# Kernel optimization log

Measured on AMD Instinct MI355X. Metric: run time of the kernel, lower is better.

Reference implementation:

```python
import jax, jax.numpy as jnp
import numpy as np

N_NODES = 100000


def gcn_conv(h, src, dst, n_nodes):
    """One GCNConv propagation with self-loops and symmetric normalization.
    h: [N, D] already linearly transformed node features.
    src, dst: [E2] int32/int64 edge endpoints (self-loops already appended).
    """
    deg = jnp.zeros((n_nodes,), h.dtype).at[dst].add(jnp.ones_like(dst, dtype=h.dtype))
    dinv = jnp.where(deg > 0, jax.lax.rsqrt(deg), 0.0)  # deg^{-1/2}, 0 for isolated
    norm = dinv[src] * dinv[dst]                         # [E2]
    msgs = norm[:, None] * h[src]                        # gather + scale
    return jnp.zeros((n_nodes, h.shape[1]), h.dtype).at[dst].add(msgs)


def setup_inputs() -> dict:
    key = jax.random.key(0)
    k1, k2, k3, k4 = jax.random.split(key, 4)
    F_IN, HID, N_CLS, N_EDGES = 512, 16, 64, 3200000
    x = jax.random.normal(k1, (N_NODES, F_IN), dtype=jnp.float32)
    edge_index = jax.random.randint(k2, (2, N_EDGES), 0, N_NODES, dtype=jnp.int64)
    W1 = jax.random.normal(k3, (F_IN, HID), dtype=jnp.float32) * (1.0 / np.sqrt(F_IN))
    b1 = jnp.zeros((HID,), jnp.float32)
    W2 = jax.random.normal(k4, (HID, N_CLS), dtype=jnp.float32) * (1.0 / np.sqrt(HID))
    b2 = jnp.zeros((N_CLS,), jnp.float32)
    return {"x": x, "edge_index": edge_index, "W1": W1, "b1": b1, "W2": W2, "b2": b2}


def reference(x, edge_index, W1, b1, W2, b2):
    n = x.shape[0]
    loops = jnp.arange(n, dtype=edge_index.dtype)
    src = jnp.concatenate([edge_index[0], loops])
    dst = jnp.concatenate([edge_index[1], loops])
    # layer 1: transform -> propagate -> bias -> relu (dropout is identity in eval)
    h = gcn_conv(x @ W1, src, dst, n) + b1
    h = jax.nn.relu(h)
    # layer 2
    out = gcn_conv(h @ W2, src, dst, n) + b2
    return out
```

## Files before the change

kernel.cpp:

```cpp
#include <hip/hip_runtime.h>

typedef unsigned short u16;
typedef unsigned int u32;

#define FIN 512
#define HID 16
#define NCLS 64

#define NBSH 7
#define BUCK (1 << NBSH)
#define SENTS ((1u << 25) - 1u)

typedef __bf16 bf16x8 __attribute__((ext_vector_type(8)));
typedef float f32x4 __attribute__((ext_vector_type(4)));

__device__ __forceinline__ float bf2f_raw(u16 u) {
    u32 x = ((u32)u) << 16;
    float f; __builtin_memcpy(&f, &x, 4); return f;
}
__device__ __forceinline__ float ldf(const void* p, long long i, int f32) {
    return f32 ? ((const float*)p)[i] : bf2f_raw(((const u16*)p)[i]);
}
__device__ __forceinline__ u16 f2bf_rne(float v) {
    u32 bits; __builtin_memcpy(&bits, &v, 4);
    u32 lsb = (bits >> 16) & 1;
    bits += 0x7FFFu + lsb;
    return (u16)(bits >> 16);
}

__global__ void k_probe(const void* x, const void* w1, const int* eidx, int E,
                        int* flags) {
    __shared__ int nz_x, nz_w, weird_x, weird_w, odd_nz;
    if (threadIdx.x == 0) { nz_x = 0; nz_w = 0; weird_x = 0; weird_w = 0; odd_nz = 0; }
    __syncthreads();
    const u16* xu = (const u16*)x;
    const u16* wu = (const u16*)w1;
    for (int i = threadIdx.x; i < 8192; i += 256) {
        u16 u = xu[i];
        if (u) atomicOr(&nz_x, 1);
        int e = (u >> 7) & 0xff;
        if ((e == 0 && (u & 0x7f)) || e >= 0xC0) atomicAdd(&weird_x, 1);
        u16 w = wu[i];
        if (w) atomicOr(&nz_w, 1);
        int ew = (w >> 7) & 0xff;
        if ((ew == 0 && (w & 0x7f)) || ew >= 0xC0) atomicAdd(&weird_w, 1);
    }
    int lim = (2 * E < 4096) ? 2 * E : 4096;
    for (int i = 1 + 2 * (int)threadIdx.x; i < lim; i += 512) {
        if (eidx[i] != 0) atomicOr(&odd_nz, 1);
    }
    __syncthreads();
    if (threadIdx.x == 0) {
        flags[0] = (odd_nz == 0) ? 1 : 0;
        flags[1] = (weird_x > 64) ? 1 : 0;
        flags[2] = (weird_w > 64) ? 1 : 0;
        flags[3] = (nz_x == 0) ? 1 : 0;
        flags[4] = (nz_w == 0) ? 1 : 0;
    }
}

__device__ __forceinline__ int ld_src(const int* eidx, int E, int e, int f64) {
    return f64 ? eidx[2LL * e] : eidx[e];
}
__device__ __forceinline__ int ld_dst(const int* eidx, int E, int e, int f64) {
    return f64 ? eidx[2LL * E + 2LL * e] : eidx[(long long)E + e];
}

__global__ void k_binA(const int* eidx, const int* flags, int* bcnt8,
                       int E, int n, int nbuck, int nblocks) {
    extern __shared__ int lcnt[];
    int tid = threadIdx.x;
    for (int i = tid; i < nbuck; i += 256) lcnt[i] = 0;
    __syncthreads();
    int f64 = flags[0];
    long long stride = (long long)nblocks * 256;
    for (long long e = (long long)blockIdx.x * 256 + tid; e < E; e += stride) {
        int d = ld_dst(eidx, E, (int)e, f64);
        if ((unsigned)d < (unsigned)n) atomicAdd(&lcnt[d >> NBSH], 1);
    }
    __syncthreads();
    int sub = blockIdx.x & 7;
    for (int i = tid; i < nbuck; i += 256) {
        int v = lcnt[i];
        if (v) atomicAdd(&bcnt8[i * 8 + sub], v);
    }
}

__global__ void k_scanb(const int* bcnt8, int* boff, int* cursor8, int NSUB) {
    __shared__ int part[1024];
    int t = threadIdx.x;
    int K = (NSUB + 1023) >> 10;
    long long base = (long long)t * K;
    int local = 0;
    for (int j = 0; j < K; j++) {
        long long idx = base + j;
        if (idx < NSUB) local += bcnt8[idx];
    }
    part[t] = local;
    __syncthreads();
    for (int s = 1; s < 1024; s <<= 1) {
        int u = (t >= s) ? part[t - s] : 0;
        __syncthreads();
        part[t] += u;
        __syncthreads();
    }
    int acc = part[t] - local;
    for (int j = 0; j < K; j++) {
        long long idx = base + j;
        if (idx < NSUB) {
            int v = bcnt8[idx];
            boff[idx] = acc;
            cursor8[idx] = acc;
            acc += v;
        }
    }
    if (t == 1023) boff[NSUB] = part[1023];
}

__global__ void k_binB(const int* eidx, const int* flags, int* cursor8,
                       u32* pairs, int E, int n, int nblocks) {
    int f64 = flags[0];
    int sub = blockIdx.x & 7;
    long long stride = (long long)nblocks * 256;
    for (long long e = (long long)blockIdx.x * 256 + threadIdx.x; e < E; e += stride) {
        int d = ld_dst(eidx, E, (int)e, f64);
        if ((unsigned)d >= (unsigned)n) continue;
        int s = ld_src(eidx, E, (int)e, f64);
        u32 su = ((unsigned)s < (unsigned)n) ? (u32)s : SENTS;
        int slot = atomicAdd(&cursor8[(d >> NBSH) * 8 + sub], 1);
        pairs[slot] = ((u32)(d & (BUCK - 1)) << 25) | su;
    }
}

__global__ void __launch_bounds__(256)
k_csrb(const u32* pairs, const int* boff, float* dinv, int* row_start,
       int* csr, int n, int nbuck) {
    __shared__ int cnt[BUCK];
    __shared__ int ex[BUCK];
    __shared__ int cur[BUCK];
    int b = blockIdx.x, tid = threadIdx.x;
    for (int i = tid; i < BUCK; i += 256) cnt[i] = 0;
    __syncthreads();
    int beg = boff[b * 8], end = boff[b * 8 + 8];
    for (int i = beg + tid; i < end; i += 256) atomicAdd(&cnt[pairs[i] >> 25], 1);
    __syncthreads();
    if (tid < BUCK) ex[tid] = cnt[tid];
    __syncthreads();
    for (int s = 1; s < BUCK; s <<= 1) {
        int u = (tid >= s && tid < BUCK) ? ex[tid - s] : 0;
        __syncthreads();
        if (tid < BUCK) ex[tid] += u;
        __syncthreads();
    }
    int base = b << NBSH;
    if (tid < BUCK) {
        int e0 = ex[tid] - cnt[tid];
        cur[tid] = e0;
        int node = base + tid;
        if (node < n) {
            row_start[node] = beg + e0;
            dinv[node] = rsqrtf((float)cnt[tid] + 1.0f);
        }
    }
    if (b == nbuck - 1 && tid == 0) row_start[n] = boff[nbuck * 8];
    __syncthreads();
    for (int i = beg + tid; i < end; i += 256) {
        u32 pr = pairs[i];
        int dl = pr >> 25;
        u32 s = pr & SENTS;
        int slot = atomicAdd(&cur[dl], 1);
        csr[beg + slot] = (s < (unsigned)n) ? (int)s : -1;
    }
}

__global__ void __launch_bounds__(256)
k_gemm1(const void* x, const void* w1, const int* flags, const float* dinv,
        float* h0s, int n) {
    __shared__ __attribute__((aligned(16))) u16 w1t[16 * 512];
    int tid = threadIdx.x;
    int fx = flags[1], fw = flags[2];
    for (int i = tid; i < 8192; i += 256) {
        int k = i >> 4, f = i & 15;
        float v = ldf(w1, (long long)k * HID + f, fw);
        int idx = ((f << 9) + k) ^ ((f & 7) << 3);
        w1t[idx] = f2bf_rne(v);
    }
    __syncthreads();

    int wave = tid >> 6;
    int lane = tid & 63;
    int base = blockIdx.x * 64 + wave * 16;
    if (base >= n) return;
    int rowA = base + (lane & 15);
    if (rowA >= n) rowA = n - 1;
    int g = lane >> 4;
    int nn = lane & 15;
    f32x4 acc = {0.0f, 0.0f, 0.0f, 0.0f};

    if (!fx) {
        const u16* xp = (const u16*)x + (long long)rowA * FIN + g * 8;
        #pragma unroll
        for (int kb = 0; kb < FIN; kb += 32) {
            bf16x8 a = *(const bf16x8*)(xp + kb);
            int bidx = ((nn << 9) + kb + g * 8) ^ ((nn & 7) << 3);
            bf16x8 b = *(const bf16x8*)(w1t + bidx);
            acc = __builtin_amdgcn_mfma_f32_16x16x32_bf16(a, b, acc, 0, 0, 0);
        }
    } else {
        const float* xp = (const float*)x + (long long)rowA * FIN + g * 8;
        #pragma unroll 4
        for (int kb = 0; kb < FIN; kb += 32) {
            float vf[8];
            *(float4*)(vf) = *(const float4*)(xp + kb);
            *(float4*)(vf + 4) = *(const float4*)(xp + kb + 4);
            bf16x8 a;
            #pragma unroll
            for (int j = 0; j < 8; j++) ((u16*)&a)[j] = f2bf_rne(vf[j]);
            int bidx = ((nn << 9) + kb + g * 8) ^ ((nn & 7) << 3);
            bf16x8 b = *(const bf16x8*)(w1t + bidx);
            acc = __builtin_amdgcn_mfma_f32_16x16x32_bf16(a, b, acc, 0, 0, 0);
        }
    }
    #pragma unroll
    for (int r = 0; r < 4; r++) {
        int node = base + g * 4 + r;
        if (node < n) h0s[node * HID + nn] = acc[r] * dinv[node];
    }
}

template <int RELU>
__global__ void k_gather(const int* row_start, const int* csr, const float* dinv,
                         const float* h_in, const void* b, const int* flags,
                         float* h_out, int n) {
    int t = blockIdx.x * 256 + threadIdx.x;
    if (t >= n * 4) return;
    int d = t >> 2;
    int g = t & 3;
    int beg = row_start[d], end = row_start[d + 1];
    const float4* hv = (const float4*)h_in;
    float4 acc = hv[d * 4 + g];
    #pragma unroll 4
    for (int i = beg; i < end; i++) {
        int s = csr[i];
        if (s >= 0) {
            float4 v = hv[s * 4 + g];
            acc.x += v.x; acc.y += v.y; acc.z += v.z; acc.w += v.w;
        }
    }
    float di = dinv[d];
    float4 o;
    if (RELU) {
        int fw = flags[2];
        o.x = di * fmaxf(di * acc.x + ldf(b, g * 4 + 0, fw), 0.0f);
        o.y = di * fmaxf(di * acc.y + ldf(b, g * 4 + 1, fw), 0.0f);
        o.z = di * fmaxf(di * acc.z + ldf(b, g * 4 + 2, fw), 0.0f);
        o.w = di * fmaxf(di * acc.w + ldf(b, g * 4 + 3, fw), 0.0f);
    } else {
        o.x = di * acc.x; o.y = di * acc.y; o.z = di * acc.z; o.w = di * acc.w;
    }
    ((float4*)h_out)[t] = o;
}

__global__ void k_check(const int* eidx, const float* h0s, const float* g,
                        int* flags, int E, int n) {
    __shared__ int h0nz, gnz, dstz;
    if (threadIdx.x == 0) { h0nz = 0; gnz = 0; dstz = 0; }
    __syncthreads();
    for (int i = threadIdx.x; i < 4096; i += 256) {
        if (h0s[i] != 0.0f) atomicOr(&h0nz, 1);
        if (g[i] != 0.0f) atomicOr(&gnz, 1);
    }
    int f64 = flags[0];
    for (int e = threadIdx.x; e < 2048; e += 256) {
        if (ld_dst(eidx, E, e, f64) == 0) atomicAdd(&dstz, 1);
    }
    __syncthreads();
    if (threadIdx.x == 0) {
        int b0 = flags[3];
        int b1 = flags[4];
        int b2 = (dstz > 102);
        int b3 = (h0nz == 0);
        int b4 = (gnz == 0);
        int b5 = flags[1];
        int b6 = flags[2];
        int b7 = flags[0];
        flags[9] = b0 | (b1 << 1) | (b2 << 2) | (b3 << 3) | (b4 << 4) |
                   (b5 << 5) | (b6 << 6) | (b7 << 7);
        flags[8] = (b0 | b1 | b2 | b3 | b4) ? 1 : 0;
    }
}

__global__ void SimplifiedGCN_5574867550498_kernel(
        const float* g, const void* w2, const void* b2, const int* flags,
        float* out, int n) {
    int t = blockIdx.x * 256 + threadIdx.x;
    if (t >= n * NCLS) return;
    int node = t >> 6;
    int c = t & 63;
    int fw = flags[2];
    float acc = ldf(b2, c, fw);
    for (int k = 0; k < HID; k++) {
        acc += g[node * HID + k] * ldf(w2, (long long)k * NCLS + c, fw);
    }
    if (t == 0 && flags[8]) acc = 4096.0f + 2.0f * (float)flags[9];
    out[t] = acc;
}

extern "C" void kernel_launch(void* const* d_in, const int* in_sizes, int n_in,
                              void* d_out, int out_size, void* d_ws, size_t ws_size,
                              hipStream_t stream) {
    const void* x = d_in[0];
    const int* eidx = (const int*)d_in[1];
    const void* w1 = d_in[2];
    const void* b1 = d_in[3];
    const void* w2 = d_in[4];
    const void* b2 = d_in[5];
    float* out = (float*)d_out;

    int n = in_sizes[0] / FIN;
    int E = in_sizes[1] / 2;
    int total_out = n * NCLS;
    int nb_out = (total_out + 255) / 256;
    size_t out_bytes = (size_t)total_out * 4;

    hipMemsetAsync(d_out, 0x42, out_bytes, stream);

    if (n <= 0 || E <= 0 || n_in < 6) {
        hipMemsetAsync(d_out, 0x4E, out_bytes, stream);
        return;
    }
    if (n >= (1 << 25)) {
        hipMemsetAsync(d_out, 0x4B, out_bytes, stream);
        return;
    }

    int nbuck = (n + BUCK - 1) >> NBSH;
    int NSUB = nbuck * 8;

    size_t A = 255;
    size_t o_flags = 0;
    size_t o_dinv  = 256;
    size_t o_h0s   = o_dinv + (((size_t)n * 4 + A) & ~A);
    size_t o_h2ps  = o_h0s  + (((size_t)n * HID * 4 + A) & ~A);
    size_t o_g     = o_h2ps + (((size_t)n * HID * 4 + A) & ~A);
    size_t o_bcnt  = o_g    + (((size_t)n * HID * 4 + A) & ~A);
    size_t o_boff  = o_bcnt + (((size_t)NSUB * 4 + A) & ~A);
    size_t o_cur   = o_boff + (((size_t)(NSUB + 1) * 4 + A) & ~A);
    size_t o_rs    = o_cur  + (((size_t)NSUB * 4 + A) & ~A);
    size_t o_pairs = o_rs   + (((size_t)(n + 1) * 4 + A) & ~A);
    size_t o_csr   = o_pairs + (((size_t)E * 4 + A) & ~A);
    size_t need    = o_csr  + (((size_t)E * 4 + A) & ~A);

    if (ws_size < need) {
        hipMemsetAsync(d_out, 0x4A, out_bytes, stream);
        return;
    }

    char* p = (char*)d_ws;
    int* flags     = (int*)(p + o_flags);
    float* dinv    = (float*)(p + o_dinv);
    float* h0s     = (float*)(p + o_h0s);
    float* h2ps    = (float*)(p + o_h2ps);
    float* g       = (float*)(p + o_g);
    int* bcnt8     = (int*)(p + o_bcnt);
    int* boff      = (int*)(p + o_boff);
    int* cursor8   = (int*)(p + o_cur);
    int* row_start = (int*)(p + o_rs);
    u32* pairs     = (u32*)(p + o_pairs);
    int* csr       = (int*)(p + o_csr);

    int nb_g1 = (n + 63) / 64;
    int nb_h4 = (n * 4 + 255) / 256;
    int nbA = 512, nbB = 1024;

    k_probe<<<1, 256, 0, stream>>>(x, w1, eidx, E, flags);
    hipMemsetAsync(bcnt8, 0, (size_t)NSUB * 4, stream);
    k_binA<<<nbA, 256, (size_t)nbuck * 4, stream>>>(eidx, flags, bcnt8, E, n,
                                                    nbuck, nbA);
    k_scanb<<<1, 1024, 0, stream>>>(bcnt8, boff, cursor8, NSUB);
    k_binB<<<nbB, 256, 0, stream>>>(eidx, flags, cursor8, pairs, E, n, nbB);
    k_csrb<<<nbuck, 256, 0, stream>>>(pairs, boff, dinv, row_start, csr, n, nbuck);
    k_gemm1<<<nb_g1, 256, 0, stream>>>(x, w1, flags, dinv, h0s, n);
    k_gather<1><<<nb_h4, 256, 0, stream>>>(row_start, csr, dinv, h0s, b1, flags,
                                           h2ps, n);
    k_gather<0><<<nb_h4, 256, 0, stream>>>(row_start, csr, dinv, h2ps, b1, flags,
                                           g, n);
    k_check<<<1, 256, 0, stream>>>(eidx, h0s, g, flags, E, n);
    SimplifiedGCN_5574867550498_kernel<<<nb_out, 256, 0, stream>>>(
        g, w2, b2, flags, out, n);
}
```

Before: 712.7 us.

## Replace global atomic bucket cursors with per-block LDS cursors and larger buckets

Edge binning now gives each block a contiguous edge range and a per-(bucket, block) count matrix, so the scan produces exact per-block offsets. Scatter then uses LDS atomics instead of contended global atomics. Buckets grow from 128 to 1024 nodes, so the CSR build runs fewer, larger blocks of 1024 threads, and the pair packing shifts to 22 source bits. The cost is a larger count matrix (about 50k entries) for the single-block scan to process, plus a lower limit on node count.

New measurement: 669.8 us. 1.06x faster.

```diff
diff --git a/kernel.cpp b/kernel.cpp
--- a/kernel.cpp
+++ b/kernel.cpp
@@ -7,9 +7,10 @@
 #define HID 16
 #define NCLS 64
 
-#define NBSH 7
+#define NBSH 10
 #define BUCK (1 << NBSH)
-#define SENTS ((1u << 25) - 1u)
+#define NBLK 512
+#define SENTS ((1u << 22) - 1u)
 
 typedef __bf16 bf16x8 __attribute__((ext_vector_type(8)));
 typedef float f32x4 __attribute__((ext_vector_type(4)));
@@ -65,28 +66,31 @@
 __device__ __forceinline__ int ld_dst(const int* eidx, int E, int e, int f64) {
     return f64 ? eidx[2LL * E + 2LL * e] : eidx[(long long)E + e];
 }
-
-__global__ void k_binA(const int* eidx, const int* flags, int* bcnt8,
-                       int E, int n, int nbuck, int nblocks) {
+__device__ __forceinline__ void blk_range(int E, int bid, int* e0, int* e1) {
+    *e0 = (int)((long long)E * bid / NBLK);
+    *e1 = (int)((long long)E * (bid + 1) / NBLK);
+}
+
+__global__ void __launch_bounds__(512)
+k_binA(const int* eidx, const int* flags, int* bcnt, int E, int n, int nbuck) {
     extern __shared__ int lcnt[];
-    int tid = threadIdx.x;
-    for (int i = tid; i < nbuck; i += 256) lcnt[i] = 0;
+    int tid = threadIdx.x, bid = blockIdx.x;
+    for (int i = tid; i < nbuck; i += 512) lcnt[i] = 0;
     __syncthreads();
     int f64 = flags[0];
-    long long stride = (long long)nblocks * 256;
-    for (long long e = (long long)blockIdx.x * 256 + tid; e < E; e += stride) {
-        int d = ld_dst(eidx, E, (int)e, f64);
+    int e0, e1; blk_range(E, bid, &e0, &e1);
+    for (int e = e0 + tid; e < e1; e += 512) {
+        int d = ld_dst(eidx, E, e, f64);
         if ((unsigned)d < (unsigned)n) atomicAdd(&lcnt[d >> NBSH], 1);
     }
     __syncthreads();
-    int sub = blockIdx.x & 7;
-    for (int i = tid; i < nbuck; i += 256) {
+    for (int i = tid; i < nbuck; i += 512) {
         int v = lcnt[i];
-        if (v) atomicAdd(&bcnt8[i * 8 + sub], v);
-    }
-}
-
-__global__ void k_scanb(const int* bcnt8, int* boff, int* cursor8, int NSUB) {
+        if (v) bcnt[(long long)i * NBLK + bid] = v;
+    }
+}
+
+__global__ void k_scanb(const int* bcnt, int* boff, int NSUB) {
     __shared__ int part[1024];
     int t = threadIdx.x;
     int K = (NSUB + 1023) >> 10;
@@ -94,7 +98,7 @@
     int local = 0;
     for (int j = 0; j < K; j++) {
         long long idx = base + j;
-        if (idx < NSUB) local += bcnt8[idx];
+        if (idx < NSUB) local += bcnt[idx];
     }
     part[t] = local;
     __syncthreads();
@@ -108,52 +112,56 @@
     for (int j = 0; j < K; j++) {
         long long idx = base + j;
         if (idx < NSUB) {
-            int v = bcnt8[idx];
+            int v = bcnt[idx];
             boff[idx] = acc;
-            cursor8[idx] = acc;
             acc += v;
         }
     }
     if (t == 1023) boff[NSUB] = part[1023];
 }
 
-__global__ void k_binB(const int* eidx, const int* flags, int* cursor8,
-                       u32* pairs, int E, int n, int nblocks) {
+__global__ void __launch_bounds__(512)
+k_binB(const int* eidx, const int* flags, const int* boff, u32* pairs,
+       int E, int n, int nbuck) {
+    extern __shared__ int lcur[];
+    int tid = threadIdx.x, bid = blockIdx.x;
+    for (int i = tid; i < nbuck; i += 512)
+        lcur[i] = boff[(long long)i * NBLK + bid];
+    __syncthreads();
     int f64 = flags[0];
-    int sub = blockIdx.x & 7;
-    long long stride = (long long)nblocks * 256;
-    for (long long e = (long long)blockIdx.x * 256 + threadIdx.x; e < E; e += stride) {
-        int d = ld_dst(eidx, E, (int)e, f64);
+    int e0, e1; blk_range(E, bid, &e0, &e1);
+    for (int e = e0 + tid; e < e1; e += 512) {
+        int d = ld_dst(eidx, E, e, f64);
         if ((unsigned)d >= (unsigned)n) continue;
-        int s = ld_src(eidx, E, (int)e, f64);
+        int s = ld_src(eidx, E, e, f64);
         u32 su = ((unsigned)s < (unsigned)n) ? (u32)s : SENTS;
-        int slot = atomicAdd(&cursor8[(d >> NBSH) * 8 + sub], 1);
-        pairs[slot] = ((u32)(d & (BUCK - 1)) << 25) | su;
-    }
-}
-
-__global__ void __launch_bounds__(256)
+        int slot = atomicAdd(&lcur[d >> NBSH], 1);
+        pairs[slot] = ((u32)(d & (BUCK - 1)) << 22) | su;
+    }
+}
+
+__global__ void __launch_bounds__(1024)
 k_csrb(const u32* pairs, const int* boff, float* dinv, int* row_start,
        int* csr, int n, int nbuck) {
     __shared__ int cnt[BUCK];
     __shared__ int ex[BUCK];
     __shared__ int cur[BUCK];
     int b = blockIdx.x, tid = threadIdx.x;
-    for (int i = tid; i < BUCK; i += 256) cnt[i] = 0;
-    __syncthreads();
-    int beg = boff[b * 8], end = boff[b * 8 + 8];
-    for (int i = beg + tid; i < end; i += 256) atomicAdd(&cnt[pairs[i] >> 25], 1);
-    __syncthreads();
-    if (tid < BUCK) ex[tid] = cnt[tid];
+    cnt[tid] = 0;
+    __syncthreads();
+    int beg = boff[(long long)b * NBLK], end = boff[(long long)(b + 1) * NBLK];
+    for (int i = beg + tid; i < end; i += 1024) atomicAdd(&cnt[pairs[i] >> 22], 1);
+    __syncthreads();
+    ex[tid] = cnt[tid];
     __syncthreads();
     for (int s = 1; s < BUCK; s <<= 1) {
-        int u = (tid >= s && tid < BUCK) ? ex[tid - s] : 0;
+        int u = (tid >= s) ? ex[tid - s] : 0;
         __syncthreads();
-        if (tid < BUCK) ex[tid] += u;
+        ex[tid] += u;
         __syncthreads();
     }
     int base = b << NBSH;
-    if (tid < BUCK) {
+    {
         int e0 = ex[tid] - cnt[tid];
         cur[tid] = e0;
         int node = base + tid;
@@ -162,11 +170,11 @@
             dinv[node] = rsqrtf((float)cnt[tid] + 1.0f);
         }
     }
-    if (b == nbuck - 1 && tid == 0) row_start[n] = boff[nbuck * 8];
-    __syncthreads();
-    for (int i = beg + tid; i < end; i += 256) {
+    if (b == nbuck - 1 && tid == 0) row_start[n] = boff[(long long)nbuck * NBLK];
+    __syncthreads();
+    for (int i = beg + tid; i < end; i += 1024) {
         u32 pr = pairs[i];
-        int dl = pr >> 25;
+        int dl = pr >> 22;
         u32 s = pr & SENTS;
         int slot = atomicAdd(&cur[dl], 1);
         csr[beg + slot] = (s < (unsigned)n) ? (int)s : -1;
@@ -329,13 +337,13 @@
         hipMemsetAsync(d_out, 0x4E, out_bytes, stream);
         return;
     }
-    if (n >= (1 << 25)) {
+    if (n >= (int)SENTS) {
         hipMemsetAsync(d_out, 0x4B, out_bytes, stream);
         return;
     }
 
     int nbuck = (n + BUCK - 1) >> NBSH;
-    int NSUB = nbuck * 8;
+    long long NSUB = (long long)nbuck * NBLK;
 
     size_t A = 255;
     size_t o_flags = 0;
@@ -345,8 +353,7 @@
     size_t o_g     = o_h2ps + (((size_t)n * HID * 4 + A) & ~A);
     size_t o_bcnt  = o_g    + (((size_t)n * HID * 4 + A) & ~A);
     size_t o_boff  = o_bcnt + (((size_t)NSUB * 4 + A) & ~A);
-    size_t o_cur   = o_boff + (((size_t)(NSUB + 1) * 4 + A) & ~A);
-    size_t o_rs    = o_cur  + (((size_t)NSUB * 4 + A) & ~A);
+    size_t o_rs    = o_boff + (((size_t)(NSUB + 1) * 4 + A) & ~A);
     size_t o_pairs = o_rs   + (((size_t)(n + 1) * 4 + A) & ~A);
     size_t o_csr   = o_pairs + (((size_t)E * 4 + A) & ~A);
     size_t need    = o_csr  + (((size_t)E * 4 + A) & ~A);
@@ -362,24 +369,22 @@
     float* h0s     = (float*)(p + o_h0s);
     float* h2ps    = (float*)(p + o_h2ps);
     float* g       = (float*)(p + o_g);
-    int* bcnt8     = (int*)(p + o_bcnt);
+    int* bcnt      = (int*)(p + o_bcnt);
     int* boff      = (int*)(p + o_boff);
-    int* cursor8   = (int*)(p + o_cur);
     int* row_start = (int*)(p + o_rs);
     u32* pairs     = (u32*)(p + o_pairs);
     int* csr       = (int*)(p + o_csr);
 
     int nb_g1 = (n + 63) / 64;
     int nb_h4 = (n * 4 + 255) / 256;
-    int nbA = 512, nbB = 1024;
+    size_t lds_bin = (size_t)nbuck * 4;
 
     k_probe<<<1, 256, 0, stream>>>(x, w1, eidx, E, flags);
-    hipMemsetAsync(bcnt8, 0, (size_t)NSUB * 4, stream);
-    k_binA<<<nbA, 256, (size_t)nbuck * 4, stream>>>(eidx, flags, bcnt8, E, n,
-                                                    nbuck, nbA);
-    k_scanb<<<1, 1024, 0, stream>>>(bcnt8, boff, cursor8, NSUB);
-    k_binB<<<nbB, 256, 0, stream>>>(eidx, flags, cursor8, pairs, E, n, nbB);
-    k_csrb<<<nbuck, 256, 0, stream>>>(pairs, boff, dinv, row_start, csr, n, nbuck);
+    hipMemsetAsync(bcnt, 0, (size_t)NSUB * 4, stream);
+    k_binA<<<NBLK, 512, lds_bin, stream>>>(eidx, flags, bcnt, E, n, nbuck);
+    k_scanb<<<1, 1024, 0, stream>>>(bcnt, boff, (int)NSUB);
+    k_binB<<<NBLK, 512, lds_bin, stream>>>(eidx, flags, boff, pairs, E, n, nbuck);
+    k_csrb<<<nbuck, 1024, 0, stream>>>(pairs, boff, dinv, row_start, csr, n, nbuck);
     k_gemm1<<<nb_g1, 256, 0, stream>>>(x, w1, flags, dinv, h0s, n);
     k_gather<1><<<nb_h4, 256, 0, stream>>>(row_start, csr, dinv, h0s, b1, flags,
                                            h2ps, n);
```
